# Kernel optimization log

Hardware: AMD Instinct MI355X
Metric: run time of the kernel (lower is better)

The kernel has to match this reference:

```python
import jax, jax.numpy as jnp
import numpy as np

B, I, O, P = 32, 2048, 64, 4  # batch, input caps, output caps, pose side
D = P * P
EPS = 1e-7
N_ITERS = 3

def setup_inputs() -> dict:
    key = jax.random.key(0)
    k1, k2, k3, k4, k5 = jax.random.split(key, 5)
    return {
        'input_poses': jax.random.normal(k1, (B, I, P, P), dtype=jnp.float32),
        'input_activations': jax.random.uniform(k2, (B, I), dtype=jnp.float32),
        'w': jax.random.normal(k3, (O, I, P, P), dtype=jnp.float32) * 0.05,
        'beta_a': jax.random.normal(k4, (1, O), dtype=jnp.float32),
        'beta_u': jax.random.normal(k5, (1, O), dtype=jnp.float32),
    }

def em_routing(V, a_in, beta_a, beta_u):
    # V: [B,O,I,D] votes, a_in: [B,I], beta_a/beta_u: [1,O]
    b, o, i, d = V.shape
    R = jnp.full((b, o, i), 1.0 / o, dtype=V.dtype)
    mu = None
    a_out = None
    for t in range(N_ITERS):
        inv_temp = 1.0 + t  # inverse temperature (lambda) schedule
        # ---- M-step ----
        r = R * a_in[:, None, :]                              # [B,O,I]
        r_sum = r.sum(axis=2, keepdims=True) + EPS            # [B,O,1]
        mu = jnp.einsum('boi,boid->bod', r, V) / r_sum        # [B,O,D]
        diff2 = (V - mu[:, :, None, :]) ** 2                  # [B,O,I,D]
        sigma2 = jnp.einsum('boi,boid->bod', r, diff2) / r_sum + EPS
        cost = (beta_u[:, :, None] + 0.5 * jnp.log(sigma2)) * r_sum  # [B,O,D]
        a_out = jax.nn.sigmoid(inv_temp * (beta_a - cost.sum(axis=-1)))  # [B,O]
        # ---- E-step ----
        if t < N_ITERS - 1:
            log_p = -0.5 * jnp.sum(diff2 / sigma2[:, :, None, :] + jnp.log(sigma2)[:, :, None, :], axis=-1)  # [B,O,I]
            R = jax.nn.softmax(jnp.log(a_out + EPS)[:, :, None] + log_p, axis=1)
    return mu, a_out

def reference(input_poses, input_activations, w, beta_a, beta_u):
    # votes: poses[B,1,I,P,P] @ w[O,I,P,P] -> [B,O,I,P,P]
    votes = jnp.einsum('bipq,oiqr->boipr', input_poses, w)
    V = votes.reshape(B, O, I, D)
    mu, a_out = em_routing(V, input_activations, beta_a, beta_u)
    capsule_poses = mu.reshape(B, O, P, P)
    return capsule_poses, a_out
```

## Files before the change

### kernel.cpp

```cpp
#include <hip/hip_runtime.h>
#include <stdint.h>

constexpr int Bn = 32, In = 2048;
constexpr float EPSF = 1e-7f;
constexpr int NC  = 64;
constexpr int IPB = In / NC;
constexpr int IPW = IPB / 4;

template <int CTRL>
__device__ __forceinline__ float dpp_add(float x) {
  int y = __builtin_amdgcn_update_dpp(0, __float_as_int(x), CTRL, 0xF, 0xF, true);
  return x + __int_as_float(y);
}

__device__ __forceinline__ float wave_sum64(float x) {
  x = dpp_add<0x121>(x);
  x = dpp_add<0x122>(x);
  x = dpp_add<0x124>(x);
  x = dpp_add<0x128>(x);
#if __has_builtin(__builtin_amdgcn_permlane16_swap)
  {
    auto pr = __builtin_amdgcn_permlane16_swap(__float_as_uint(x), __float_as_uint(x), false, false);
    x = __uint_as_float(pr[0]) + __uint_as_float(pr[1]);
  }
#else
  x += __int_as_float(__builtin_amdgcn_ds_swizzle(__float_as_int(x), 0x401F));
#endif
#if __has_builtin(__builtin_amdgcn_permlane32_swap)
  {
    auto pr = __builtin_amdgcn_permlane32_swap(__float_as_uint(x), __float_as_uint(x), false, false);
    x = __uint_as_float(pr[0]) + __uint_as_float(pr[1]);
  }
#else
  x += __shfl_xor(x, 32);
#endif
  return x;
}

__global__ __launch_bounds__(256) void transpose_w_k(const float4* __restrict__ w,
                                                     float4* __restrict__ w_t) {
  int idx = blockIdx.x * 256 + threadIdx.x;
  int o = idx >> 13;
  int rest = idx & 8191;
  int i = rest >> 2;
  int k = rest & 3;
  w_t[(size_t)((i << 2) + k) * 64 + o] = w[idx];
}

template <int TPASS>
__global__ __launch_bounds__(256, 4) void pass_k(const float* __restrict__ poses,
                                                 const float* __restrict__ a_in,
                                                 const float* __restrict__ w_t,
                                                 const float* __restrict__ params,
                                                 float* __restrict__ partials) {
  const int gid = blockIdx.x;
  const int xcd = gid & 7;
  const int s   = gid >> 3;
  const int b   = s & 31;
  const int cc  = xcd * 8 + (s >> 5);
  const int tid = threadIdx.x, wv = tid >> 6, ln = tid & 63;
  const int i0 = cc * IPB + wv * IPW;

  float mu[16], hs[16], c0 = 0.f;
  if (TPASS > 0) {
    const float4* pp4 = (const float4*)(params + (size_t)(b * 64 + ln) * 36);
#pragma unroll
    for (int k = 0; k < 4; ++k) {
      float4 v = pp4[k];
      mu[4 * k] = v.x; mu[4 * k + 1] = v.y; mu[4 * k + 2] = v.z; mu[4 * k + 3] = v.w;
    }
#pragma unroll
    for (int k = 0; k < 4; ++k) {
      float4 v = pp4[4 + k];
      hs[4 * k] = v.x; hs[4 * k + 1] = v.y; hs[4 * k + 2] = v.z; hs[4 * k + 3] = v.w;
    }
    c0 = ((const float*)pp4)[32];
  }

  float rs = 0.f, S1[16], S2[16];
#pragma unroll
  for (int d = 0; d < 16; ++d) { S1[d] = 0.f; S2[d] = 0.f; }

  const float4* wt4 = (const float4*)w_t;
  const float4* po4 = (const float4*)poses;

#pragma unroll
  for (int ii = 0; ii < IPW; ++ii) {
    const int i = i0 + ii;
    float4 w0 = wt4[(size_t)(i * 4 + 0) * 64 + ln];
    float4 w1 = wt4[(size_t)(i * 4 + 1) * 64 + ln];
    float4 w2 = wt4[(size_t)(i * 4 + 2) * 64 + ln];
    float4 w3 = wt4[(size_t)(i * 4 + 3) * 64 + ln];
    const float4* pp = po4 + ((size_t)b * In + i) * 4;
    float4 p0 = pp[0], p1 = pp[1], p2 = pp[2], p3 = pp[3];
    float V[16];
#define VROW(p, Pv)                                                              \
    V[p * 4 + 0] = fmaf(Pv.w, w3.x, fmaf(Pv.z, w2.x, fmaf(Pv.y, w1.x, Pv.x * w0.x))); \
    V[p * 4 + 1] = fmaf(Pv.w, w3.y, fmaf(Pv.z, w2.y, fmaf(Pv.y, w1.y, Pv.x * w0.y))); \
    V[p * 4 + 2] = fmaf(Pv.w, w3.z, fmaf(Pv.z, w2.z, fmaf(Pv.y, w1.z, Pv.x * w0.z))); \
    V[p * 4 + 3] = fmaf(Pv.w, w3.w, fmaf(Pv.z, w2.w, fmaf(Pv.y, w1.w, Pv.x * w0.w)));
    VROW(0, p0) VROW(1, p1) VROW(2, p2) VROW(3, p3)
#undef VROW
    const float a = a_in[(size_t)b * In + i];
    float r;
    if (TPASS == 0) {
      r = a * 0.015625f;
    } else {
      float u0 = c0, u1 = 0.f, u2 = 0.f, u3 = 0.f;
#pragma unroll
      for (int j = 0; j < 4; ++j) {
        float d0 = V[j] - mu[j];           u0 = fmaf(-d0 * d0, hs[j], u0);
        float d1 = V[4 + j] - mu[4 + j];   u1 = fmaf(-d1 * d1, hs[4 + j], u1);
        float d2 = V[8 + j] - mu[8 + j];   u2 = fmaf(-d2 * d2, hs[8 + j], u2);
        float d3 = V[12 + j] - mu[12 + j]; u3 = fmaf(-d3 * d3, hs[12 + j], u3);
      }
      float u = (u0 + u1) + (u2 + u3);
      float e = __expf(u);
      float ss = wave_sum64(e) + 1e-37f;
      r = a * e * __builtin_amdgcn_rcpf(ss);
    }
    rs += r;
#pragma unroll
    for (int d = 0; d < 16; ++d) {
      float t1 = r * V[d];
      S1[d] += t1;
      S2[d] = fmaf(t1, V[d], S2[d]);
    }
  }

  __shared__ float lds[4][33][64];
  lds[wv][0][ln] = rs;
#pragma unroll
  for (int d = 0; d < 16; ++d) {
    lds[wv][1 + d][ln] = S1[d];
    lds[wv][17 + d][ln] = S2[d];
  }
  __syncthreads();
  for (int idx = tid; idx < 33 * 64; idx += 256) {
    int j = idx >> 6, o = idx & 63;
    float ssum = lds[0][j][o] + lds[1][j][o] + lds[2][j][o] + lds[3][j][o];
    partials[((size_t)(b * NC + cc) * 33 + j) * 64 + o] = ssum;
  }
}

__global__ __launch_bounds__(256) void red_k(const float* __restrict__ partials,
                                             float* __restrict__ red) {
  const int idx = blockIdx.x * 256 + threadIdx.x;
  const int b = idx / 2112;
  const int rr = idx - b * 2112;
  const float* base = partials + (size_t)b * NC * 2112 + rr;
  float s = 0.f;
#pragma unroll 8
  for (int c = 0; c < NC; ++c) s += base[(size_t)c * 2112];
  red[idx] = s;
}

template <int TPASS>
__global__ __launch_bounds__(256) void fin_k(const float* __restrict__ red,
                                             const float* __restrict__ beta_a,
                                             const float* __restrict__ beta_u,
                                             float* __restrict__ params,
                                             float* __restrict__ out) {
  const int g = blockIdx.x * 256 + threadIdx.x;
  const int b = g >> 6, o = g & 63;
  const float* base = red + (size_t)b * 2112 + o;
  const float r_sum = base[0] + EPSF;
  const float inv = 1.f / r_sum;
  float muv[16], sg[16], lsum = 0.f;
#pragma unroll
  for (int d = 0; d < 16; ++d) {
    float m = base[(1 + d) * 64] * inv;
    float s2 = fmaxf(base[(17 + d) * 64] * inv - m * m, 0.f) + EPSF;
    muv[d] = m; sg[d] = s2; lsum += logf(s2);
  }
  const float cost = (16.f * beta_u[o] + 0.5f * lsum) * r_sum;
  const float aout = 1.f / (1.f + __expf(-(float)(TPASS + 1) * (beta_a[o] - cost)));
  if (TPASS < 2) {
    float c0 = logf(aout + EPSF) - 0.5f * lsum;
    float mx = c0;
#pragma unroll
    for (int k = 1; k < 64; k <<= 1) mx = fmaxf(mx, __shfl_xor(mx, k));
    float* pp = params + (size_t)g * 36;
#pragma unroll
    for (int d = 0; d < 16; ++d) {
      pp[d] = muv[d];
      pp[16 + d] = 0.5f / sg[d];
    }
    pp[32] = c0 - mx;
  } else {
#pragma unroll
    for (int d = 0; d < 16; ++d) out[(size_t)g * 16 + d] = muv[d];
    out[Bn * 64 * 16 + g] = aout;
  }
}

extern "C" void kernel_launch(void* const* d_in, const int* in_sizes, int n_in,
                              void* d_out, int out_size, void* d_ws, size_t ws_size,
                              hipStream_t stream) {
  const float* poses  = (const float*)d_in[0];
  const float* a_in   = (const float*)d_in[1];
  const float* w      = (const float*)d_in[2];
  const float* beta_a = (const float*)d_in[3];
  const float* beta_u = (const float*)d_in[4];
  float* out = (float*)d_out;

  float* w_t      = (float*)d_ws;
  float* partials = w_t + (size_t)In * 64 * 16;
  float* red      = partials + (size_t)Bn * NC * 33 * 64;
  float* params   = red + (size_t)Bn * 33 * 64;

  transpose_w_k<<<dim3(In * 64 * 4 / 256), 256, 0, stream>>>((const float4*)w, (float4*)w_t);

  dim3 pg(Bn * NC);
  dim3 rg(Bn * 33 * 64 / 256);
  pass_k<0><<<pg, 256, 0, stream>>>(poses, a_in, w_t, params, partials);
  red_k<<<rg, 256, 0, stream>>>(partials, red);
  fin_k<0><<<Bn * 64 / 256, 256, 0, stream>>>(red, beta_a, beta_u, params, out);
  pass_k<1><<<pg, 256, 0, stream>>>(poses, a_in, w_t, params, partials);
  red_k<<<rg, 256, 0, stream>>>(partials, red);
  fin_k<1><<<Bn * 64 / 256, 256, 0, stream>>>(red, beta_a, beta_u, params, out);
  pass_k<2><<<pg, 256, 0, stream>>>(poses, a_in, w_t, params, partials);
  red_k<<<rg, 256, 0, stream>>>(partials, red);
  fin_k<2><<<Bn * 64 / 256, 256, 0, stream>>>(red, beta_a, beta_u, params, out);
}
```

Baseline: 191.7 us.

## Replace partials buffer and reduction kernel with global atomic accumulation

Each wave in the pass kernel now atomically adds its per-output sums directly into the reduced buffer, removing the LDS cross-wave reduction, the partials array and the separate reduction kernel. The buffer is zeroed with a memset before each pass. This removes the large partials write/read traffic and a kernel launch per iteration, but issues many contended float atomics and makes the summation order nondeterministic.

```diff
diff --git a/kernel.cpp b/kernel.cpp
--- a/kernel.cpp
+++ b/kernel.cpp
@@ -52,7 +52,7 @@
                                                  const float* __restrict__ a_in,
                                                  const float* __restrict__ w_t,
                                                  const float* __restrict__ params,
-                                                 float* __restrict__ partials) {
+                                                 float* __restrict__ red) {
   const int gid = blockIdx.x;
   const int xcd = gid & 7;
   const int s   = gid >> 3;
@@ -128,31 +128,13 @@
     }
   }
 
-  __shared__ float lds[4][33][64];
-  lds[wv][0][ln] = rs;
+  float* rp = red + (size_t)b * 2112 + ln;
+  atomicAdd(rp, rs);
 #pragma unroll
   for (int d = 0; d < 16; ++d) {
-    lds[wv][1 + d][ln] = S1[d];
-    lds[wv][17 + d][ln] = S2[d];
-  }
-  __syncthreads();
-  for (int idx = tid; idx < 33 * 64; idx += 256) {
-    int j = idx >> 6, o = idx & 63;
-    float ssum = lds[0][j][o] + lds[1][j][o] + lds[2][j][o] + lds[3][j][o];
-    partials[((size_t)(b * NC + cc) * 33 + j) * 64 + o] = ssum;
-  }
-}
-
-__global__ __launch_bounds__(256) void red_k(const float* __restrict__ partials,
-                                             float* __restrict__ red) {
-  const int idx = blockIdx.x * 256 + threadIdx.x;
-  const int b = idx / 2112;
-  const int rr = idx - b * 2112;
-  const float* base = partials + (size_t)b * NC * 2112 + rr;
-  float s = 0.f;
-#pragma unroll 8
-  for (int c = 0; c < NC; ++c) s += base[(size_t)c * 2112];
-  red[idx] = s;
+    atomicAdd(rp + (1 + d) * 64, S1[d]);
+    atomicAdd(rp + (17 + d) * 64, S2[d]);
+  }
 }
 
 template <int TPASS>
@@ -204,22 +186,24 @@
   const float* beta_u = (const float*)d_in[4];
   float* out = (float*)d_out;
 
-  float* w_t      = (float*)d_ws;
-  float* partials = w_t + (size_t)In * 64 * 16;
-  float* red      = partials + (size_t)Bn * NC * 33 * 64;
-  float* params   = red + (size_t)Bn * 33 * 64;
+  float* w_t    = (float*)d_ws;
+  float* red    = w_t + (size_t)In * 64 * 16;
+  float* params = red + (size_t)Bn * 33 * 64;
 
   transpose_w_k<<<dim3(In * 64 * 4 / 256), 256, 0, stream>>>((const float4*)w, (float4*)w_t);
 
+  const size_t red_bytes = (size_t)Bn * 33 * 64 * sizeof(float);
   dim3 pg(Bn * NC);
-  dim3 rg(Bn * 33 * 64 / 256);
-  pass_k<0><<<pg, 256, 0, stream>>>(poses, a_in, w_t, params, partials);
-  red_k<<<rg, 256, 0, stream>>>(partials, red);
+
+  hipMemsetAsync(red, 0, red_bytes, stream);
+  pass_k<0><<<pg, 256, 0, stream>>>(poses, a_in, w_t, params, red);
   fin_k<0><<<Bn * 64 / 256, 256, 0, stream>>>(red, beta_a, beta_u, params, out);
-  pass_k<1><<<pg, 256, 0, stream>>>(poses, a_in, w_t, params, partials);
-  red_k<<<rg, 256, 0, stream>>>(partials, red);
+
+  hipMemsetAsync(red, 0, red_bytes, stream);
+  pass_k<1><<<pg, 256, 0, stream>>>(poses, a_in, w_t, params, red);
   fin_k<1><<<Bn * 64 / 256, 256, 0, stream>>>(red, beta_a, beta_u, params, out);
-  pass_k<2><<<pg, 256, 0, stream>>>(poses, a_in, w_t, params, partials);
-  red_k<<<rg, 256, 0, stream>>>(partials, red);
+
+  hipMemsetAsync(red, 0, red_bytes, stream);
+  pass_k<2><<<pg, 256, 0, stream>>>(poses, a_in, w_t, params, red);
   fin_k<2><<<Bn * 64 / 256, 256, 0, stream>>>(red, beta_a, beta_u, params, out);
 }
```

Result: slower. 285.4 us (+48.9%).
